# Optimization experiments

Measured on AMD Instinct MI355X. Metric: run time of the kernel, lower is better.

Reference implementation:

```python
import jax, jax.numpy as jnp
import numpy as np

NUM_HEADS = 16


def setup_inputs() -> dict:
    key = jax.random.key(0)
    k1, k2, k3 = jax.random.split(key, 3)
    B, S, D = 4, 2048, 1024
    x = jax.random.normal(k1, (B, S, D), dtype=jnp.float32)
    w_qkv = jax.random.normal(k2, (D, 3 * D), dtype=jnp.float32) * 0.02
    b_qkv = jnp.zeros((3 * D,), dtype=jnp.float32)
    w_proj = jax.random.normal(k3, (D, D), dtype=jnp.float32) * 0.02
    b_proj = jnp.zeros((D,), dtype=jnp.float32)
    return {"x": x, "w_qkv": w_qkv, "b_qkv": b_qkv, "w_proj": w_proj, "b_proj": b_proj}


def reference(x, w_qkv, b_qkv, w_proj, b_proj):
    B, S, D = x.shape
    H = NUM_HEADS
    hd = D // H
    # fused qkv projection: [B,S,3D] -> [B,S,3H,hd]
    qkv = (x @ w_qkv + b_qkv).reshape(B, S, 3 * H, hd)
    q, k, v = jnp.split(qkv, 3, axis=2)  # each [B,S,H,hd]
    scale = (1.0 / jnp.sqrt(hd)).astype(x.dtype)
    scores = jnp.einsum("bqhd,bkhd->bhqk", q, k) * scale  # [B,H,S,S]
    causal = jnp.tril(jnp.ones((S, S), dtype=bool))  # [S,S]
    masked = jnp.where(causal, scores, jnp.finfo(scores.dtype).min)
    # softmax in fp32 reduce dtype, cast back (dropout_rate=0 -> identity)
    attn = jax.nn.softmax(masked.astype(jnp.float32)).astype(masked.dtype)
    out = jnp.einsum("bhqk,bkhd->bqhd", attn, v).reshape(B, S, D)
    return out @ w_proj + b_proj
```

## Files before the change

kernel.cpp:

```cpp
#include <hip/hip_runtime.h>
#include <hip/hip_bf16.h>

typedef __attribute__((ext_vector_type(8))) short short8;
typedef __attribute__((ext_vector_type(4))) float f32x4;

#define B_   4
#define S_   2048
#define D_   1024
#define H_   16
#define HD_  64
#define M_   (B_ * S_)
#define N3_  (3 * D_)

#define GLDS16(g, l)                                                        \
  __builtin_amdgcn_global_load_lds(                                         \
      (const __attribute__((address_space(1))) void*)(g),                   \
      (__attribute__((address_space(3))) void*)(l), 16, 0, 0)

__device__ __forceinline__ unsigned pack_bf2(float a, float b) {
  union { __hip_bfloat16 h; unsigned short s; } ua, ub;
  ua.h = __float2bfloat16(a);
  ub.h = __float2bfloat16(b);
  return (unsigned)ua.s | ((unsigned)ub.s << 16);
}

__global__ __launch_bounds__(256) void cast_f32_bf16(
    const float* __restrict__ in, __hip_bfloat16* __restrict__ out, int n) {
  int i = (blockIdx.x * 256 + threadIdx.x) * 4;
  if (i + 3 < n) {
    float4 v = *(const float4*)(in + i);
    union { ushort4 u4; __hip_bfloat16 h[4]; } p;
    p.h[0] = __float2bfloat16(v.x);
    p.h[1] = __float2bfloat16(v.y);
    p.h[2] = __float2bfloat16(v.z);
    p.h[3] = __float2bfloat16(v.w);
    *(ushort4*)(out + i) = p.u4;
  }
}

__global__ __launch_bounds__(256) void transpose_cast(
    const float* __restrict__ in, __hip_bfloat16* __restrict__ out,
    int rows, int cols) {
  __shared__ float tile[32][33];
  int bx = blockIdx.x * 32;
  int by = blockIdx.y * 32;
  int tx = threadIdx.x, ty = threadIdx.y;
#pragma unroll
  for (int i = 0; i < 4; ++i)
    tile[ty + i * 8][tx] = in[(size_t)(by + ty + i * 8) * cols + bx + tx];
  __syncthreads();
#pragma unroll
  for (int i = 0; i < 4; ++i)
    out[(size_t)(bx + ty + i * 8) * rows + by + tx] =
        __float2bfloat16(tile[tx][ty + i * 8]);
}

__device__ inline void store_out(float* p, float v) { *p = v; }
__device__ inline void store_out(__hip_bfloat16* p, float v) {
  *p = __float2bfloat16(v);
}

template <typename OUT_T, bool WVT>
__global__ __launch_bounds__(256) void gemm_bt_bias(
    const __hip_bfloat16* __restrict__ A, const __hip_bfloat16* __restrict__ Bt,
    const float* __restrict__ bias, OUT_T* __restrict__ C,
    __hip_bfloat16* __restrict__ vt, int M, int N, int K) {
  __shared__ __align__(16) __hip_bfloat16 Alds[128 * 64];
  __shared__ __align__(16) __hip_bfloat16 Blds[128 * 64];
  const int t = threadIdx.x;
  const int wave = t >> 6, lane = t & 63;
  const int quad = lane >> 4, l15 = lane & 15;
  const int wm = (wave >> 1) * 64, wn = (wave & 1) * 64;
  const int m0 = blockIdx.y * 128, n0 = blockIdx.x * 128;

  const int rsub = lane >> 3;
  const int gc16 = (lane & 7) ^ (rsub & 7);
  const __hip_bfloat16* gA[4];
  const __hip_bfloat16* gB[4];
  __hip_bfloat16* lA[4];
  __hip_bfloat16* lB[4];
#pragma unroll
  for (int i = 0; i < 4; ++i) {
    int c = wave * 4 + i;
    int row = c * 8 + rsub;
    gA[i] = A + (size_t)(m0 + row) * K + gc16 * 8;
    gB[i] = Bt + (size_t)(n0 + row) * K + gc16 * 8;
    lA[i] = Alds + c * 512;
    lB[i] = Blds + c * 512;
  }

  f32x4 acc[4][4] = {};

  for (int k0 = 0; k0 < K; k0 += 64) {
#pragma unroll
    for (int i = 0; i < 4; ++i) {
      GLDS16(gA[i] + k0, lA[i]);
      GLDS16(gB[i] + k0, lB[i]);
    }
    __syncthreads();
#pragma unroll
    for (int kk = 0; kk < 2; ++kk) {
      const int fo = ((kk * 4 + quad) ^ (l15 & 7)) * 8;
      short8 a[4], bfr[4];
#pragma unroll
      for (int mt = 0; mt < 4; ++mt)
        a[mt] = *(const short8*)(Alds + (wm + mt * 16 + l15) * 64 + fo);
#pragma unroll
      for (int nt = 0; nt < 4; ++nt)
        bfr[nt] = *(const short8*)(Blds + (wn + nt * 16 + l15) * 64 + fo);
#pragma unroll
      for (int mt = 0; mt < 4; ++mt)
#pragma unroll
        for (int nt = 0; nt < 4; ++nt)
          acc[mt][nt] = __builtin_amdgcn_mfma_f32_16x16x32_bf16(
              a[mt], bfr[nt], acc[mt][nt], 0, 0, 0);
    }
    __syncthreads();
  }

  if (WVT && n0 >= 2048) {
#pragma unroll
    for (int mt = 0; mt < 4; ++mt)
#pragma unroll
      for (int nt = 0; nt < 4; ++nt) {
        int col = n0 + wn + nt * 16 + l15;
        float bv = bias[col];
        int hv = (col - 2048) >> 6, d = (col - 2048) & 63;
        int row0 = m0 + wm + mt * 16 + quad * 4;
        int bidx = row0 >> 11, s = row0 & 2047;
        uint2 w;
        w.x = pack_bf2(acc[mt][nt][0] + bv, acc[mt][nt][1] + bv);
        w.y = pack_bf2(acc[mt][nt][2] + bv, acc[mt][nt][3] + bv);
        *(uint2*)(vt + ((size_t)(bidx * 16 + hv) * 64 + d) * 2048 + s) = w;
      }
  } else {
#pragma unroll
    for (int mt = 0; mt < 4; ++mt)
#pragma unroll
      for (int nt = 0; nt < 4; ++nt) {
        int col = n0 + wn + nt * 16 + l15;
        float bv = bias[col];
#pragma unroll
        for (int r = 0; r < 4; ++r) {
          int row = m0 + wm + mt * 16 + quad * 4 + r;
          store_out(C + (size_t)row * N + col, acc[mt][nt][r] + bv);
        }
      }
  }
}

__global__ __launch_bounds__(256) void attn_causal(
    const __hip_bfloat16* __restrict__ qkv,
    const __hip_bfloat16* __restrict__ vt,
    __hip_bfloat16* __restrict__ ctx) {
  __shared__ __align__(16) __hip_bfloat16 Klds[64][72];
  __shared__ __align__(16) __hip_bfloat16 Vlds[64][72];
  __shared__ __align__(16) __hip_bfloat16 Plds[4][16][72];

  const int t = threadIdx.x;
  const int wave = t >> 6, lane = t & 63;
  const int quad = lane >> 4, l15 = lane & 15;
  const int xb = blockIdx.x, h = blockIdx.y, b = blockIdx.z;

  const size_t qbase = (size_t)b * S_ * N3_ + h * HD_;
  const size_t kbase = qbase + D_;
  const size_t vtbase = (size_t)(b * H_ + h) * HD_ * S_;
  const float C2 = 0.18033688f;

  short8 ones;
#pragma unroll
  for (int j = 0; j < 8; ++j) ones[j] = (short)0x3F80;

  for (int sel = 0; sel < 2; ++sel) {
    const int qb = sel ? (31 - xb) : xb;
    const int qrow = qb * 64 + wave * 16 + l15;
    short8 qf0 = *(const short8*)(qkv + qbase + (size_t)qrow * N3_ + quad * 8);
    short8 qf1 =
        *(const short8*)(qkv + qbase + (size_t)qrow * N3_ + 32 + quad * 8);

    f32x4 o[4] = {};
    float m_r = -1e30f, l_r = 0.f;

    for (int kb = 0; kb <= qb; ++kb) {
#pragma unroll
      for (int i = 0; i < 2; ++i) {
        int c = t + 256 * i;
        int row = c >> 3, seg = c & 7;
        *(uint4*)(&Klds[row][seg * 8]) = *(const uint4*)(
            qkv + kbase + (size_t)(kb * 64 + row) * N3_ + seg * 8);
        *(uint4*)(&Vlds[row][seg * 8]) = *(const uint4*)(
            vt + vtbase + (size_t)row * S_ + kb * 64 + seg * 8);
      }
      __syncthreads();

      f32x4 st[4];
#pragma unroll
      for (int nt = 0; nt < 4; ++nt) {
        f32x4 z = {};
        short8 k0 = *(const short8*)(&Klds[nt * 16 + l15][quad * 8]);
        short8 k1 = *(const short8*)(&Klds[nt * 16 + l15][32 + quad * 8]);
        z = __builtin_amdgcn_mfma_f32_16x16x32_bf16(k0, qf0, z, 0, 0, 0);
        z = __builtin_amdgcn_mfma_f32_16x16x32_bf16(k1, qf1, z, 0, 0, 0);
        st[nt] = z;
      }
      if (kb == qb) {
        const int rloc = wave * 16 + l15;
#pragma unroll
        for (int nt = 0; nt < 4; ++nt)
#pragma unroll
          for (int r = 0; r < 4; ++r)
            if (nt * 16 + quad * 4 + r > rloc) st[nt][r] = -1e30f;
      }

      float tm = st[0][0];
#pragma unroll
      for (int nt = 0; nt < 4; ++nt)
#pragma unroll
        for (int r = 0; r < 4; ++r) tm = fmaxf(tm, st[nt][r]);
      tm = fmaxf(tm, __shfl_xor(tm, 16));
      tm = fmaxf(tm, __shfl_xor(tm, 32));
      const float mn = fmaxf(m_r, tm * C2);
      const float alpha = __builtin_amdgcn_exp2f(m_r - mn);
      m_r = mn;

#pragma unroll
      for (int nt = 0; nt < 4; ++nt) {
        float p0 = __builtin_amdgcn_exp2f(__builtin_fmaf(st[nt][0], C2, -mn));
        float p1 = __builtin_amdgcn_exp2f(__builtin_fmaf(st[nt][1], C2, -mn));
        float p2 = __builtin_amdgcn_exp2f(__builtin_fmaf(st[nt][2], C2, -mn));
        float p3 = __builtin_amdgcn_exp2f(__builtin_fmaf(st[nt][3], C2, -mn));
        uint2 w;
        w.x = pack_bf2(p0, p1);
        w.y = pack_bf2(p2, p3);
        *(uint2*)(&Plds[wave][l15][nt * 16 + quad * 4]) = w;
      }

#pragma unroll
      for (int dt = 0; dt < 4; ++dt)
#pragma unroll
        for (int r = 0; r < 4; ++r) o[dt][r] *= alpha;

      short8 pB0 = *(const short8*)(&Plds[wave][l15][quad * 8]);
      short8 pB1 = *(const short8*)(&Plds[wave][l15][32 + quad * 8]);

      f32x4 ps = {};
      ps = __builtin_amdgcn_mfma_f32_16x16x32_bf16(ones, pB0, ps, 0, 0, 0);
      ps = __builtin_amdgcn_mfma_f32_16x16x32_bf16(ones, pB1, ps, 0, 0, 0);
      l_r = alpha * l_r + ps[0];

#pragma unroll
      for (int dt = 0; dt < 4; ++dt) {
        short8 v0 = *(const short8*)(&Vlds[dt * 16 + l15][quad * 8]);
        short8 v1 = *(const short8*)(&Vlds[dt * 16 + l15][32 + quad * 8]);
        o[dt] = __builtin_amdgcn_mfma_f32_16x16x32_bf16(v0, pB0, o[dt], 0, 0, 0);
        o[dt] = __builtin_amdgcn_mfma_f32_16x16x32_bf16(v1, pB1, o[dt], 0, 0, 0);
      }
      __syncthreads();
    }

    const float rl = __builtin_amdgcn_rcpf(l_r);
    __hip_bfloat16* crow = ctx + ((size_t)b * S_ + qrow) * D_ + h * HD_;
#pragma unroll
    for (int dt = 0; dt < 4; ++dt) {
      uint2 w;
      w.x = pack_bf2(o[dt][0] * rl, o[dt][1] * rl);
      w.y = pack_bf2(o[dt][2] * rl, o[dt][3] * rl);
      *(uint2*)(crow + dt * 16 + quad * 4) = w;
    }
  }
}

extern "C" void kernel_launch(void* const* d_in, const int* in_sizes, int n_in,
                              void* d_out, int out_size, void* d_ws,
                              size_t ws_size, hipStream_t stream) {
  const float* x      = (const float*)d_in[0];
  const float* w_qkv  = (const float*)d_in[1];
  const float* b_qkv  = (const float*)d_in[2];
  const float* w_proj = (const float*)d_in[3];
  const float* b_proj = (const float*)d_in[4];
  float* out = (float*)d_out;

  char* ws = (char*)d_ws;
  __hip_bfloat16* xb     = (__hip_bfloat16*)(ws + 0);
  __hip_bfloat16* vtb    = (__hip_bfloat16*)(ws + 0);
  __hip_bfloat16* wqkvT  = (__hip_bfloat16*)(ws + 16777216);
  __hip_bfloat16* wprojT = (__hip_bfloat16*)(ws + 23068672);
  __hip_bfloat16* qkvb   = (__hip_bfloat16*)(ws + 25165824);
  __hip_bfloat16* ctx    = (__hip_bfloat16*)(ws + 75497472);
  __hip_bfloat16* vt2    = (__hip_bfloat16*)(ws + 91750400);

  cast_f32_bf16<<<8192, 256, 0, stream>>>(x, xb, M_ * D_);
  transpose_cast<<<dim3(N3_ / 32, D_ / 32), dim3(32, 8), 0, stream>>>(
      w_qkv, wqkvT, D_, N3_);
  transpose_cast<<<dim3(D_ / 32, D_ / 32), dim3(32, 8), 0, stream>>>(
      w_proj, wprojT, D_, D_);

  gemm_bt_bias<__hip_bfloat16, true>
      <<<dim3(N3_ / 128, M_ / 128), 256, 0, stream>>>(
          xb, wqkvT, b_qkv, qkvb, vt2, M_, N3_, D_);

  attn_causal<<<dim3(16, H_, B_), 256, 0, stream>>>(qkvb, vt2, ctx);

  gemm_bt_bias<float, false><<<dim3(D_ / 128, M_ / 128), 256, 0, stream>>>(
      ctx, wprojT, b_proj, out, (__hip_bfloat16*)nullptr, M_, D_, D_);
}
```

Baseline: 289.6 us.

## Give each attention wave two 16-row query groups to reuse K/V fragments

```diff
diff --git a/kernel.cpp b/kernel.cpp
--- a/kernel.cpp
+++ b/kernel.cpp
@@ -149,13 +149,13 @@
   }
 }
 
-__global__ __launch_bounds__(256) void attn_causal(
+__global__ __launch_bounds__(128) void attn_causal(
     const __hip_bfloat16* __restrict__ qkv,
     const __hip_bfloat16* __restrict__ vt,
     __hip_bfloat16* __restrict__ ctx) {
   __shared__ __align__(16) __hip_bfloat16 Klds[64][72];
   __shared__ __align__(16) __hip_bfloat16 Vlds[64][72];
-  __shared__ __align__(16) __hip_bfloat16 Plds[4][16][72];
+  __shared__ __align__(16) __hip_bfloat16 Plds[2][2][16][72];
 
   const int t = threadIdx.x;
   const int wave = t >> 6, lane = t & 63;
@@ -173,18 +173,23 @@
 
   for (int sel = 0; sel < 2; ++sel) {
     const int qb = sel ? (31 - xb) : xb;
-    const int qrow = qb * 64 + wave * 16 + l15;
-    short8 qf0 = *(const short8*)(qkv + qbase + (size_t)qrow * N3_ + quad * 8);
-    short8 qf1 =
-        *(const short8*)(qkv + qbase + (size_t)qrow * N3_ + 32 + quad * 8);
-
-    f32x4 o[4] = {};
-    float m_r = -1e30f, l_r = 0.f;
+    short8 qf[2][2];
+#pragma unroll
+    for (int g = 0; g < 2; ++g) {
+      const int qrow = qb * 64 + wave * 32 + g * 16 + l15;
+      qf[g][0] =
+          *(const short8*)(qkv + qbase + (size_t)qrow * N3_ + quad * 8);
+      qf[g][1] =
+          *(const short8*)(qkv + qbase + (size_t)qrow * N3_ + 32 + quad * 8);
+    }
+
+    f32x4 o[2][4] = {};
+    float m_r[2] = {-1e30f, -1e30f}, l_r[2] = {0.f, 0.f};
 
     for (int kb = 0; kb <= qb; ++kb) {
 #pragma unroll
-      for (int i = 0; i < 2; ++i) {
-        int c = t + 256 * i;
+      for (int i = 0; i < 4; ++i) {
+        int c = t + 128 * i;
         int row = c >> 3, seg = c & 7;
         *(uint4*)(&Klds[row][seg * 8]) = *(const uint4*)(
             qkv + kbase + (size_t)(kb * 64 + row) * N3_ + seg * 8);
@@ -193,79 +198,103 @@
       }
       __syncthreads();
 
-      f32x4 st[4];
+      short8 kf[4][2];
 #pragma unroll
       for (int nt = 0; nt < 4; ++nt) {
-        f32x4 z = {};
-        short8 k0 = *(const short8*)(&Klds[nt * 16 + l15][quad * 8]);
-        short8 k1 = *(const short8*)(&Klds[nt * 16 + l15][32 + quad * 8]);
-        z = __builtin_amdgcn_mfma_f32_16x16x32_bf16(k0, qf0, z, 0, 0, 0);
-        z = __builtin_amdgcn_mfma_f32_16x16x32_bf16(k1, qf1, z, 0, 0, 0);
-        st[nt] = z;
-      }
-      if (kb == qb) {
-        const int rloc = wave * 16 + l15;
+        kf[nt][0] = *(const short8*)(&Klds[nt * 16 + l15][quad * 8]);
+        kf[nt][1] = *(const short8*)(&Klds[nt * 16 + l15][32 + quad * 8]);
+      }
+
+      const bool diag = (kb == qb);
+#pragma unroll
+      for (int g = 0; g < 2; ++g) {
+        f32x4 st[4];
+#pragma unroll
+        for (int nt = 0; nt < 4; ++nt) {
+          f32x4 z = {};
+          z = __builtin_amdgcn_mfma_f32_16x16x32_bf16(kf[nt][0], qf[g][0], z,
+                                                      0, 0, 0);
+          z = __builtin_amdgcn_mfma_f32_16x16x32_bf16(kf[nt][1], qf[g][1], z,
+                                                      0, 0, 0);
+          st[nt] = z;
+        }
+        if (diag) {
+          const int rloc = wave * 32 + g * 16 + l15;
+#pragma unroll
+          for (int nt = 0; nt < 4; ++nt)
+#pragma unroll
+            for (int r = 0; r < 4; ++r)
+              if (nt * 16 + quad * 4 + r > rloc) st[nt][r] = -1e30f;
+        }
+
+        float tm = st[0][0];
 #pragma unroll
         for (int nt = 0; nt < 4; ++nt)
 #pragma unroll
-          for (int r = 0; r < 4; ++r)
-            if (nt * 16 + quad * 4 + r > rloc) st[nt][r] = -1e30f;
-      }
-
-      float tm = st[0][0];
-#pragma unroll
-      for (int nt = 0; nt < 4; ++nt)
-#pragma unroll
-        for (int r = 0; r < 4; ++r) tm = fmaxf(tm, st[nt][r]);
-      tm = fmaxf(tm, __shfl_xor(tm, 16));
-      tm = fmaxf(tm, __shfl_xor(tm, 32));
-      const float mn = fmaxf(m_r, tm * C2);
-      const float alpha = __builtin_amdgcn_exp2f(m_r - mn);
-      m_r = mn;
-
-#pragma unroll
-      for (int nt = 0; nt < 4; ++nt) {
-        float p0 = __builtin_amdgcn_exp2f(__builtin_fmaf(st[nt][0], C2, -mn));
-        float p1 = __builtin_amdgcn_exp2f(__builtin_fmaf(st[nt][1], C2, -mn));
-        float p2 = __builtin_amdgcn_exp2f(__builtin_fmaf(st[nt][2], C2, -mn));
-        float p3 = __builtin_amdgcn_exp2f(__builtin_fmaf(st[nt][3], C2, -mn));
-        uint2 w;
-        w.x = pack_bf2(p0, p1);
-        w.y = pack_bf2(p2, p3);
-        *(uint2*)(&Plds[wave][l15][nt * 16 + quad * 4]) = w;
-      }
-
-#pragma unroll
-      for (int dt = 0; dt < 4; ++dt)
-#pragma unroll
-        for (int r = 0; r < 4; ++r) o[dt][r] *= alpha;
-
-      short8 pB0 = *(const short8*)(&Plds[wave][l15][quad * 8]);
-      short8 pB1 = *(const short8*)(&Plds[wave][l15][32 + quad * 8]);
-
-      f32x4 ps = {};
-      ps = __builtin_amdgcn_mfma_f32_16x16x32_bf16(ones, pB0, ps, 0, 0, 0);
-      ps = __builtin_amdgcn_mfma_f32_16x16x32_bf16(ones, pB1, ps, 0, 0, 0);
-      l_r = alpha * l_r + ps[0];
+          for (int r = 0; r < 4; ++r) tm = fmaxf(tm, st[nt][r]);
+        tm = fmaxf(tm, __shfl_xor(tm, 16));
+        tm = fmaxf(tm, __shfl_xor(tm, 32));
+        const float mn = fmaxf(m_r[g], tm * C2);
+        const float alpha = __builtin_amdgcn_exp2f(m_r[g] - mn);
+        m_r[g] = mn;
+        l_r[g] *= alpha;
+
+#pragma unroll
+        for (int nt = 0; nt < 4; ++nt) {
+          float p0 = __builtin_amdgcn_exp2f(__builtin_fmaf(st[nt][0], C2, -mn));
+          float p1 = __builtin_amdgcn_exp2f(__builtin_fmaf(st[nt][1], C2, -mn));
+          float p2 = __builtin_amdgcn_exp2f(__builtin_fmaf(st[nt][2], C2, -mn));
+          float p3 = __builtin_amdgcn_exp2f(__builtin_fmaf(st[nt][3], C2, -mn));
+          uint2 w;
+          w.x = pack_bf2(p0, p1);
+          w.y = pack_bf2(p2, p3);
+          *(uint2*)(&Plds[wave][g][l15][nt * 16 + quad * 4]) = w;
+        }
+
+#pragma unroll
+        for (int dt = 0; dt < 4; ++dt)
+#pragma unroll
+          for (int r = 0; r < 4; ++r) o[g][dt][r] *= alpha;
+      }
+
+      short8 pB[2][2];
+#pragma unroll
+      for (int g = 0; g < 2; ++g) {
+        pB[g][0] = *(const short8*)(&Plds[wave][g][l15][quad * 8]);
+        pB[g][1] = *(const short8*)(&Plds[wave][g][l15][32 + quad * 8]);
+        f32x4 ps = {};
+        ps = __builtin_amdgcn_mfma_f32_16x16x32_bf16(ones, pB[g][0], ps, 0, 0, 0);
+        ps = __builtin_amdgcn_mfma_f32_16x16x32_bf16(ones, pB[g][1], ps, 0, 0, 0);
+        l_r[g] += ps[0];
+      }
 
 #pragma unroll
       for (int dt = 0; dt < 4; ++dt) {
         short8 v0 = *(const short8*)(&Vlds[dt * 16 + l15][quad * 8]);
         short8 v1 = *(const short8*)(&Vlds[dt * 16 + l15][32 + quad * 8]);
-        o[dt] = __builtin_amdgcn_mfma_f32_16x16x32_bf16(v0, pB0, o[dt], 0, 0, 0);
-        o[dt] = __builtin_amdgcn_mfma_f32_16x16x32_bf16(v1, pB1, o[dt], 0, 0, 0);
+#pragma unroll
+        for (int g = 0; g < 2; ++g) {
+          o[g][dt] = __builtin_amdgcn_mfma_f32_16x16x32_bf16(v0, pB[g][0],
+                                                             o[g][dt], 0, 0, 0);
+          o[g][dt] = __builtin_amdgcn_mfma_f32_16x16x32_bf16(v1, pB[g][1],
+                                                             o[g][dt], 0, 0, 0);
+        }
       }
       __syncthreads();
     }
 
-    const float rl = __builtin_amdgcn_rcpf(l_r);
-    __hip_bfloat16* crow = ctx + ((size_t)b * S_ + qrow) * D_ + h * HD_;
-#pragma unroll
-    for (int dt = 0; dt < 4; ++dt) {
-      uint2 w;
-      w.x = pack_bf2(o[dt][0] * rl, o[dt][1] * rl);
-      w.y = pack_bf2(o[dt][2] * rl, o[dt][3] * rl);
-      *(uint2*)(crow + dt * 16 + quad * 4) = w;
+#pragma unroll
+    for (int g = 0; g < 2; ++g) {
+      const float rl = __builtin_amdgcn_rcpf(l_r[g]);
+      const int qrow = qb * 64 + wave * 32 + g * 16 + l15;
+      __hip_bfloat16* crow = ctx + ((size_t)b * S_ + qrow) * D_ + h * HD_;
+#pragma unroll
+      for (int dt = 0; dt < 4; ++dt) {
+        uint2 w;
+        w.x = pack_bf2(o[g][dt][0] * rl, o[g][dt][1] * rl);
+        w.y = pack_bf2(o[g][dt][2] * rl, o[g][dt][3] * rl);
+        *(uint2*)(crow + dt * 16 + quad * 4) = w;
+      }
     }
   }
 }
@@ -282,7 +311,6 @@
 
   char* ws = (char*)d_ws;
   __hip_bfloat16* xb     = (__hip_bfloat16*)(ws + 0);
-  __hip_bfloat16* vtb    = (__hip_bfloat16*)(ws + 0);
   __hip_bfloat16* wqkvT  = (__hip_bfloat16*)(ws + 16777216);
   __hip_bfloat16* wprojT = (__hip_bfloat16*)(ws + 23068672);
   __hip_bfloat16* qkvb   = (__hip_bfloat16*)(ws + 25165824);
@@ -299,7 +327,7 @@
       <<<dim3(N3_ / 128, M_ / 128), 256, 0, stream>>>(
           xb, wqkvT, b_qkv, qkvb, vt2, M_, N3_, D_);
 
-  attn_causal<<<dim3(16, H_, B_), 256, 0, stream>>>(qkvb, vt2, ctx);
+  attn_causal<<<dim3(16, H_, B_), 128, 0, stream>>>(qkvb, vt2, ctx);
 
   gemm_bt_bias<float, false><<<dim3(D_ / 128, M_ / 128), 256, 0, stream>>>(
       ctx, wprojT, b_proj, out, (__hip_bfloat16*)nullptr, M_, D_, D_);
```

Result: no change. 285.2 us (-1.5%).
